# Optimization experiments

Hardware: AMD Instinct MI355X
Metric: run time of the kernel (lower is better)

## Reference

```python
import jax, jax.numpy as jnp
import numpy as np

N, C = 16384, 512

def setup_inputs() -> dict:
    key = jax.random.key(0)
    k1, k2 = jax.random.split(key)
    mean = jax.random.normal(k1, (N, C), dtype=jnp.float32)
    var = jax.random.uniform(k2, (N, C), dtype=jnp.float32)  # positive diagonal variances
    return {"mean": mean, "var": var, "num_samples": 400}

def reference(mean, var, num_samples):
    # Monte Carlo estimate of E[softmax(mean + eps)], eps ~ N(0, diag(var)).
    # lax.scan keeps memory flat (no [S, N, C] buffer), matching the torch loop.
    std = jnp.sqrt(var)
    keys = jax.random.split(jax.random.key(42), num_samples)

    def body(acc, k):
        eps = jax.random.normal(k, mean.shape, dtype=mean.dtype) * std
        return acc + jax.nn.softmax(mean + eps, axis=-1), None

    acc, _ = jax.lax.scan(body, jnp.zeros_like(mean), keys)
    return acc / num_samples
```

## Files before the change

### kernel.cpp

```cpp
#include <hip/hip_runtime.h>
#include <stdint.h>

#define NSAMP 400
#define NC 512

#if __has_builtin(__builtin_amdgcn_exp2f)
#define EXP2F(x) __builtin_amdgcn_exp2f(x)
#else
#define EXP2F(x) __expf((x) * 0.6931471805599453f)
#endif
#if __has_builtin(__builtin_amdgcn_logf)
#define LOG2F(x) __builtin_amdgcn_logf(x)
#else
#define LOG2F(x) (__logf(x) * 1.4426950408889634f)
#endif

static __device__ __forceinline__ uint32_t rotl32(uint32_t v, int n) {
  return (v << n) | (v >> (32 - n));
}

static __device__ __forceinline__ void threefry2x32(
    uint32_t k0, uint32_t k1, uint32_t x0, uint32_t x1,
    uint32_t& o0, uint32_t& o1)
{
  const uint32_t ks2 = k0 ^ k1 ^ 0x1BD11BDAu;
  x0 += k0; x1 += k1;

  x0 += x1; x1 = rotl32(x1, 13); x1 ^= x0;
  x0 += x1; x1 = rotl32(x1, 15); x1 ^= x0;
  x0 += x1; x1 = rotl32(x1, 26); x1 ^= x0;
  x0 += x1; x1 = rotl32(x1,  6); x1 ^= x0;
  x0 += k1; x1 += ks2 + 1u;

  x0 += x1; x1 = rotl32(x1, 17); x1 ^= x0;
  x0 += x1; x1 = rotl32(x1, 29); x1 ^= x0;
  x0 += x1; x1 = rotl32(x1, 16); x1 ^= x0;
  x0 += x1; x1 = rotl32(x1, 24); x1 ^= x0;
  x0 += ks2; x1 += k0 + 2u;

  x0 += x1; x1 = rotl32(x1, 13); x1 ^= x0;
  x0 += x1; x1 = rotl32(x1, 15); x1 ^= x0;
  x0 += x1; x1 = rotl32(x1, 26); x1 ^= x0;
  x0 += x1; x1 = rotl32(x1,  6); x1 ^= x0;
  x0 += k0; x1 += k1 + 3u;

  x0 += x1; x1 = rotl32(x1, 17); x1 ^= x0;
  x0 += x1; x1 = rotl32(x1, 29); x1 ^= x0;
  x0 += x1; x1 = rotl32(x1, 16); x1 ^= x0;
  x0 += x1; x1 = rotl32(x1, 24); x1 ^= x0;
  x0 += k1; x1 += ks2 + 4u;

  x0 += x1; x1 = rotl32(x1, 13); x1 ^= x0;
  x0 += x1; x1 = rotl32(x1, 15); x1 ^= x0;
  x0 += x1; x1 = rotl32(x1, 26); x1 ^= x0;
  x0 += x1; x1 = rotl32(x1,  6); x1 ^= x0;
  x0 += ks2; x1 += k0 + 5u;

  o0 = x0; o1 = x1;
}

static __device__ __forceinline__ uint32_t tf_bits(uint32_t k0, uint32_t k1, uint32_t cnt) {
  uint32_t y0, y1;
  threefry2x32(k0, k1, 0u, cnt, y0, y1);
  return y0 ^ y1;
}

static __device__ __forceinline__ float softexp(float u, float L, float sd2, float m2) {
  float p;
  if (L > -7.2134752f) {
    float w = fmaf(L, -0.69314718f, -2.5f);
    p =              2.81022636e-08f;
    p = fmaf(p, w,   3.43273939e-07f);
    p = fmaf(p, w,  -3.5233877e-06f);
    p = fmaf(p, w,  -4.39150654e-06f);
    p = fmaf(p, w,   0.00021858087f);
    p = fmaf(p, w,  -0.00125372503f);
    p = fmaf(p, w,  -0.00417768164f);
    p = fmaf(p, w,   0.246640727f);
    p = fmaf(p, w,   1.50140941f);
  } else {
    float w = __builtin_amdgcn_sqrtf(L * -0.69314718f) - 3.0f;
    p =             -0.000200214257f;
    p = fmaf(p, w,   0.000100950558f);
    p = fmaf(p, w,   0.00134934322f);
    p = fmaf(p, w,  -0.00367342844f);
    p = fmaf(p, w,   0.00573950773f);
    p = fmaf(p, w,  -0.0076224613f);
    p = fmaf(p, w,   0.00943887047f);
    p = fmaf(p, w,   1.00167406f);
    p = fmaf(p, w,   2.83297682f);
  }
  float px = p * u;
  return EXP2F(fmaf(px, sd2, m2));
}

__global__ __launch_bounds__(256)
__attribute__((amdgpu_waves_per_eu(4, 4)))
void mc_softmax_kernel(const float* __restrict__ mean,
                       const float* __restrict__ var,
                       float* __restrict__ out)
{
  const int lane  = threadIdx.x & 63;
  const int row   = (blockIdx.x << 2) + (threadIdx.x >> 6);
  const int cbase = lane << 2;

  const float* mr = mean + (size_t)row * NC;
  const float* vr = var  + (size_t)row * NC;

  float m2[8], sd2[8], acc[8];
  {
    const float L2E = 1.4426950408889634f;
    const float S2L = 2.0402788959f;
    float4 t0 = *(const float4*)(mr + cbase);
    float4 t1 = *(const float4*)(mr + 256 + cbase);
    m2[0] = t0.x * L2E; m2[1] = t0.y * L2E; m2[2] = t0.z * L2E; m2[3] = t0.w * L2E;
    m2[4] = t1.x * L2E; m2[5] = t1.y * L2E; m2[6] = t1.z * L2E; m2[7] = t1.w * L2E;
    float4 v0 = *(const float4*)(vr + cbase);
    float4 v1 = *(const float4*)(vr + 256 + cbase);
    sd2[0] = __builtin_amdgcn_sqrtf(v0.x) * S2L;
    sd2[1] = __builtin_amdgcn_sqrtf(v0.y) * S2L;
    sd2[2] = __builtin_amdgcn_sqrtf(v0.z) * S2L;
    sd2[3] = __builtin_amdgcn_sqrtf(v0.w) * S2L;
    sd2[4] = __builtin_amdgcn_sqrtf(v1.x) * S2L;
    sd2[5] = __builtin_amdgcn_sqrtf(v1.y) * S2L;
    sd2[6] = __builtin_amdgcn_sqrtf(v1.z) * S2L;
    sd2[7] = __builtin_amdgcn_sqrtf(v1.w) * S2L;
  }
#pragma unroll
  for (int j = 0; j < 8; ++j) acc[j] = 0.0f;

  const uint32_t base = (uint32_t)(row * NC + cbase);
  const float lo = -0.99999994f;

  for (int s = 0; s < NSAMP; s += 2) {
    uint32_t a0, a1, b0, b1;
    threefry2x32(0u, 42u, 0u, (uint32_t)s,       a0, a1);
    threefry2x32(0u, 42u, 0u, (uint32_t)(s + 1), b0, b1);

    float uA[8], LA[8], uB[8], LB[8];
#pragma unroll
    for (int j = 0; j < 8; ++j) {
      const uint32_t cnt = base + (uint32_t)(j < 4 ? j : 252 + j);
      {
        uint32_t bits = tf_bits(a0, a1, cnt);
        float f = __uint_as_float(__builtin_amdgcn_alignbit(0x7Fu, bits, 9u)) - 1.0f;
        float u = fmaf(f, 2.0f, lo);
        uA[j] = u;
        LA[j] = LOG2F(fmaf(u, -u, 1.0f));
      }
      {
        uint32_t bits = tf_bits(b0, b1, cnt);
        float f = __uint_as_float(__builtin_amdgcn_alignbit(0x7Fu, bits, 9u)) - 1.0f;
        float u = fmaf(f, 2.0f, lo);
        uB[j] = u;
        LB[j] = LOG2F(fmaf(u, -u, 1.0f));
      }
    }

    float eA[8], eB[8], sumA = 0.0f, sumB = 0.0f;
#pragma unroll
    for (int j = 0; j < 8; ++j) {
      eA[j] = softexp(uA[j], LA[j], sd2[j], m2[j]); sumA += eA[j];
      eB[j] = softexp(uB[j], LB[j], sd2[j], m2[j]); sumB += eB[j];
    }

#pragma unroll
    for (int off = 32; off >= 1; off >>= 1) {
      sumA += __shfl_xor(sumA, off);
      sumB += __shfl_xor(sumB, off);
    }
    const float invA = __builtin_amdgcn_rcpf(sumA);
    const float invB = __builtin_amdgcn_rcpf(sumB);
#pragma unroll
    for (int j = 0; j < 8; ++j)
      acc[j] = fmaf(eA[j], invA, fmaf(eB[j], invB, acc[j]));
  }

  float* orow = out + (size_t)row * NC;
  const float sc = 1.0f / (float)NSAMP;
  float4 o0, o1;
  o0.x = acc[0] * sc; o0.y = acc[1] * sc; o0.z = acc[2] * sc; o0.w = acc[3] * sc;
  o1.x = acc[4] * sc; o1.y = acc[5] * sc; o1.z = acc[6] * sc; o1.w = acc[7] * sc;
  *(float4*)(orow + cbase)       = o0;
  *(float4*)(orow + 256 + cbase) = o1;
}

extern "C" void kernel_launch(void* const* d_in, const int* in_sizes, int n_in,
                              void* d_out, int out_size, void* d_ws, size_t ws_size,
                              hipStream_t stream) {
  const float* mean = (const float*)d_in[0];
  const float* var  = (const float*)d_in[1];
  float* out        = (float*)d_out;

  const int rows = out_size / NC;
  const int blocks = rows / 4;
  mc_softmax_kernel<<<blocks, 256, 0, stream>>>(mean, var, out);
}
```

Baseline: 7.260 ms.

## Use alignbit rotates in threefry, hoist ks2, and process one sample per iteration

Rewrites the per-element threefry hash so rotations use v_alignbit, the ks2 key schedule is computed once per sample, and the zero x0 input is folded away. The sample loop goes from two samples per iteration to one, and the fixed waves-per-EU attribute is dropped so the compiler picks register use and occupancy itself. The aim is fewer ALU instructions in the integer-heavy RNG path. Processing one sample at a time gives up some of the instruction-level parallelism and the paired shuffle reductions of the two-sample version.

```diff
diff --git a/kernel.cpp b/kernel.cpp
--- a/kernel.cpp
+++ b/kernel.cpp
@@ -16,53 +16,60 @@
 #endif
 
 static __device__ __forceinline__ uint32_t rotl32(uint32_t v, int n) {
+  return __builtin_amdgcn_alignbit(v, v, 32u - (uint32_t)n);
+}
+static __device__ __forceinline__ uint32_t rotl32_s(uint32_t v, int n) {
   return (v << n) | (v >> (32 - n));
 }
 
-static __device__ __forceinline__ void threefry2x32(
+#define TF_ROUND(x0, x1, R, ROT) \
+  x0 += x1; x1 = ROT(x1, R); x1 ^= x0;
+
+static __device__ __forceinline__ void threefry2x32_s(
     uint32_t k0, uint32_t k1, uint32_t x0, uint32_t x1,
     uint32_t& o0, uint32_t& o1)
 {
   const uint32_t ks2 = k0 ^ k1 ^ 0x1BD11BDAu;
   x0 += k0; x1 += k1;
-
-  x0 += x1; x1 = rotl32(x1, 13); x1 ^= x0;
-  x0 += x1; x1 = rotl32(x1, 15); x1 ^= x0;
-  x0 += x1; x1 = rotl32(x1, 26); x1 ^= x0;
-  x0 += x1; x1 = rotl32(x1,  6); x1 ^= x0;
+  TF_ROUND(x0,x1,13,rotl32_s) TF_ROUND(x0,x1,15,rotl32_s)
+  TF_ROUND(x0,x1,26,rotl32_s) TF_ROUND(x0,x1, 6,rotl32_s)
   x0 += k1; x1 += ks2 + 1u;
-
-  x0 += x1; x1 = rotl32(x1, 17); x1 ^= x0;
-  x0 += x1; x1 = rotl32(x1, 29); x1 ^= x0;
-  x0 += x1; x1 = rotl32(x1, 16); x1 ^= x0;
-  x0 += x1; x1 = rotl32(x1, 24); x1 ^= x0;
+  TF_ROUND(x0,x1,17,rotl32_s) TF_ROUND(x0,x1,29,rotl32_s)
+  TF_ROUND(x0,x1,16,rotl32_s) TF_ROUND(x0,x1,24,rotl32_s)
   x0 += ks2; x1 += k0 + 2u;
-
-  x0 += x1; x1 = rotl32(x1, 13); x1 ^= x0;
-  x0 += x1; x1 = rotl32(x1, 15); x1 ^= x0;
-  x0 += x1; x1 = rotl32(x1, 26); x1 ^= x0;
-  x0 += x1; x1 = rotl32(x1,  6); x1 ^= x0;
+  TF_ROUND(x0,x1,13,rotl32_s) TF_ROUND(x0,x1,15,rotl32_s)
+  TF_ROUND(x0,x1,26,rotl32_s) TF_ROUND(x0,x1, 6,rotl32_s)
   x0 += k0; x1 += k1 + 3u;
-
-  x0 += x1; x1 = rotl32(x1, 17); x1 ^= x0;
-  x0 += x1; x1 = rotl32(x1, 29); x1 ^= x0;
-  x0 += x1; x1 = rotl32(x1, 16); x1 ^= x0;
-  x0 += x1; x1 = rotl32(x1, 24); x1 ^= x0;
+  TF_ROUND(x0,x1,17,rotl32_s) TF_ROUND(x0,x1,29,rotl32_s)
+  TF_ROUND(x0,x1,16,rotl32_s) TF_ROUND(x0,x1,24,rotl32_s)
   x0 += k1; x1 += ks2 + 4u;
-
-  x0 += x1; x1 = rotl32(x1, 13); x1 ^= x0;
-  x0 += x1; x1 = rotl32(x1, 15); x1 ^= x0;
-  x0 += x1; x1 = rotl32(x1, 26); x1 ^= x0;
-  x0 += x1; x1 = rotl32(x1,  6); x1 ^= x0;
+  TF_ROUND(x0,x1,13,rotl32_s) TF_ROUND(x0,x1,15,rotl32_s)
+  TF_ROUND(x0,x1,26,rotl32_s) TF_ROUND(x0,x1, 6,rotl32_s)
   x0 += ks2; x1 += k0 + 5u;
-
   o0 = x0; o1 = x1;
 }
 
-static __device__ __forceinline__ uint32_t tf_bits(uint32_t k0, uint32_t k1, uint32_t cnt) {
-  uint32_t y0, y1;
-  threefry2x32(k0, k1, 0u, cnt, y0, y1);
-  return y0 ^ y1;
+static __device__ __forceinline__ uint32_t tf_bits(
+    uint32_t k0, uint32_t k1, uint32_t ks2, uint32_t cnt)
+{
+  uint32_t x0 = k0;
+  uint32_t x1 = cnt + k1;
+  TF_ROUND(x0,x1,13,rotl32) TF_ROUND(x0,x1,15,rotl32)
+  TF_ROUND(x0,x1,26,rotl32) TF_ROUND(x0,x1, 6,rotl32)
+  x0 += k1; x1 += ks2 + 1u;
+  TF_ROUND(x0,x1,17,rotl32) TF_ROUND(x0,x1,29,rotl32)
+  TF_ROUND(x0,x1,16,rotl32) TF_ROUND(x0,x1,24,rotl32)
+  x0 += ks2; x1 += k0 + 2u;
+  TF_ROUND(x0,x1,13,rotl32) TF_ROUND(x0,x1,15,rotl32)
+  TF_ROUND(x0,x1,26,rotl32) TF_ROUND(x0,x1, 6,rotl32)
+  x0 += k0; x1 += k1 + 3u;
+  TF_ROUND(x0,x1,17,rotl32) TF_ROUND(x0,x1,29,rotl32)
+  TF_ROUND(x0,x1,16,rotl32) TF_ROUND(x0,x1,24,rotl32)
+  x0 += k1; x1 += ks2 + 4u;
+  TF_ROUND(x0,x1,13,rotl32) TF_ROUND(x0,x1,15,rotl32)
+  TF_ROUND(x0,x1,26,rotl32) TF_ROUND(x0,x1, 6,rotl32)
+  x0 += ks2; x1 += k0 + 5u;
+  return x0 ^ x1;
 }
 
 static __device__ __forceinline__ float softexp(float u, float L, float sd2, float m2) {
@@ -95,7 +102,6 @@
 }
 
 __global__ __launch_bounds__(256)
-__attribute__((amdgpu_waves_per_eu(4, 4)))
 void mc_softmax_kernel(const float* __restrict__ mean,
                        const float* __restrict__ var,
                        float* __restrict__ out)
@@ -132,48 +138,36 @@
   const uint32_t base = (uint32_t)(row * NC + cbase);
   const float lo = -0.99999994f;
 
-  for (int s = 0; s < NSAMP; s += 2) {
-    uint32_t a0, a1, b0, b1;
-    threefry2x32(0u, 42u, 0u, (uint32_t)s,       a0, a1);
-    threefry2x32(0u, 42u, 0u, (uint32_t)(s + 1), b0, b1);
+  for (int s = 0; s < NSAMP; ++s) {
+    uint32_t k0, k1;
+    threefry2x32_s(0u, 42u, 0u, (uint32_t)s, k0, k1);
+    const uint32_t ks2 = k0 ^ k1 ^ 0x1BD11BDAu;
 
-    float uA[8], LA[8], uB[8], LB[8];
+    float u8[8], L8[8];
 #pragma unroll
     for (int j = 0; j < 8; ++j) {
       const uint32_t cnt = base + (uint32_t)(j < 4 ? j : 252 + j);
-      {
-        uint32_t bits = tf_bits(a0, a1, cnt);
-        float f = __uint_as_float(__builtin_amdgcn_alignbit(0x7Fu, bits, 9u)) - 1.0f;
-        float u = fmaf(f, 2.0f, lo);
-        uA[j] = u;
-        LA[j] = LOG2F(fmaf(u, -u, 1.0f));
-      }
-      {
-        uint32_t bits = tf_bits(b0, b1, cnt);
-        float f = __uint_as_float(__builtin_amdgcn_alignbit(0x7Fu, bits, 9u)) - 1.0f;
-        float u = fmaf(f, 2.0f, lo);
-        uB[j] = u;
-        LB[j] = LOG2F(fmaf(u, -u, 1.0f));
-      }
+      uint32_t bits = tf_bits(k0, k1, ks2, cnt);
+      float f = __uint_as_float(__builtin_amdgcn_alignbit(0x7Fu, bits, 9u)) - 1.0f;
+      float u = fmaf(f, 2.0f, lo);
+      u8[j] = u;
+      L8[j] = LOG2F(fmaf(u, -u, 1.0f));
     }
 
-    float eA[8], eB[8], sumA = 0.0f, sumB = 0.0f;
+    float e8[8], sum = 0.0f;
 #pragma unroll
     for (int j = 0; j < 8; ++j) {
-      eA[j] = softexp(uA[j], LA[j], sd2[j], m2[j]); sumA += eA[j];
-      eB[j] = softexp(uB[j], LB[j], sd2[j], m2[j]); sumB += eB[j];
+      e8[j] = softexp(u8[j], L8[j], sd2[j], m2[j]);
+      sum += e8[j];
     }
 
 #pragma unroll
-    for (int off = 32; off >= 1; off >>= 1) {
-      sumA += __shfl_xor(sumA, off);
-      sumB += __shfl_xor(sumB, off);
-    }
-    const float invA = __builtin_amdgcn_rcpf(sumA);
-    const float invB = __builtin_amdgcn_rcpf(sumB);
+    for (int off = 32; off >= 1; off >>= 1)
+      sum += __shfl_xor(sum, off);
+    const float inv = __builtin_amdgcn_rcpf(sum);
 #pragma unroll
     for (int j = 0; j < 8; ++j)
-      acc[j] = fmaf(eA[j], invA, fmaf(eB[j], invB, acc[j]));
+      acc[j] = fmaf(e8[j], inv, acc[j]);
   }
 
   float* orow = out + (size_t)row * NC;
```

Result: no change. 7.257 ms (-0.0%).
